# Kernel tuning notes

Measured on AMD Instinct MI355X. Metric: run time of the kernel, lower is better.

The kernel has to match this reference:

```python
import jax, jax.numpy as jnp
import numpy as np

# Module config (matches init_kwargs shape_data=[8,32,32], pow=1, spde_type='adv_diff')
N_T, N_Y, N_X = 8, 32, 32
N = N_Y * N_X            # nb_nodes
DX = DY = DT = 1.0


def build_A(kappa, m1, m2, h11, h12, h22):
    """Dense [N,N] advection-diffusion operator A = kappa^2 I + m.grad - div(H grad),
    central differences on the n_y x n_x grid, zero-Dirichlet boundary (9-pt stencil).
    All coefficient inputs are [N] vectors (node-wise)."""
    ii, jj = jnp.divmod(jnp.arange(N), N_X)   # ii: y index, jj: x index
    rows = jnp.arange(N)
    A = jnp.zeros((N, N), dtype=kappa.dtype)
    # center
    A = A.at[rows, rows].add(kappa ** 2 + 2.0 * h11 / DX**2 + 2.0 * h22 / DY**2)

    def add(A, di, dj, coef):
        vi, vj = ii + di, jj + dj
        valid = (vi >= 0) & (vi < N_Y) & (vj >= 0) & (vj < N_X)
        cols = jnp.clip(vi, 0, N_Y - 1) * N_X + jnp.clip(vj, 0, N_X - 1)
        return A.at[rows, cols].add(jnp.where(valid, coef, 0.0))

    A = add(A, 0, +1, -h11 / DX**2 + m1 / (2.0 * DX))
    A = add(A, 0, -1, -h11 / DX**2 - m1 / (2.0 * DX))
    A = add(A, +1, 0, -h22 / DY**2 + m2 / (2.0 * DY))
    A = add(A, -1, 0, -h22 / DY**2 - m2 / (2.0 * DY))
    cxy = h12 / (2.0 * DX * DY)    # cross term -2*H12*u_xy with /(4 dx dy) stencil
    A = add(A, +1, +1, -cxy)
    A = add(A, -1, -1, -cxy)
    A = add(A, +1, -1, +cxy)
    A = add(A, -1, +1, +cxy)
    return A


def _forward(kappa, m, H, tau):
    n_b = kappa.shape[0]
    # reorder field params to [n_b, n_t, N]
    kap = jnp.moveaxis(kappa[:, 0], -1, 1)
    m1 = jnp.moveaxis(m[:, 0], -1, 1)
    m2 = jnp.moveaxis(m[:, 1], -1, 1)
    h11 = jnp.moveaxis(H[:, 0, 0], -1, 1)
    h12 = jnp.moveaxis(H[:, 0, 1], -1, 1)
    h22 = jnp.moveaxis(H[:, 1, 1], -1, 1)
    tau_ = jnp.moveaxis(tau[:, 0], -1, 1)

    flat = lambda a: a.reshape(n_b * N_T, N)
    A = jax.vmap(build_A)(flat(kap), flat(m1), flat(m2), flat(h11), flat(h12), flat(h22))
    A = A.reshape(n_b, N_T, N, N)                 # B = A since pow == 1

    eye = jnp.eye(N, dtype=A.dtype)
    M = eye + DT * A                               # inv_M_k = I + dt*B_k, [n_b,n_t,N,N]
    w = DT / (tau_ ** 2)                           # Qs_tilde_k = diag(dt / tau_k^2)

    WM = w[..., :, None] * M                       # diag(w_k) @ M_k
    P = jnp.einsum('btij,btik->btjk', M, WM)       # M_k^T diag(w_k) M_k

    # diagonal blocks: D_k = P_k + diag(w_{k+1}) for k < n_t-1; D_{n_t-1} = P_{n_t-1}
    w_next = jnp.concatenate([w[:, 1:], jnp.zeros_like(w[:, :1])], axis=1)
    D = P + w_next[..., :, None] * eye

    # sub-diagonal block (k, k-1) = -M_k^T diag(w_k), k = 1..n_t-1 (0-block padded at front)
    zblk = jnp.zeros((n_b, 1, N, N), dtype=A.dtype)
    lower = jnp.concatenate([zblk, -jnp.swapaxes(WM[:, 1:], -1, -2)], axis=1)
    # super-diagonal block (k, k+1) = -diag(w_{k+1}) M_{k+1}, k = 0..n_t-2 (0-block at end)
    upper = jnp.concatenate([-WM[:, 1:], zblk], axis=1)

    # block-tridiagonal precision Q, packed as [n_b, 3(diag,lower,upper), n_t, N, N]
    return jnp.stack([D, lower, upper], axis=1)


def setup_inputs() -> dict:
    key = jax.random.key(0)
    ks = jax.random.split(key, 4)
    n_b = 2
    kappa = 0.1 + 0.9 * jax.random.uniform(ks[0], (n_b, 1, N, N_T), dtype=jnp.float32)
    m = 0.2 * jax.random.normal(ks[1], (n_b, 2, N, N_T), dtype=jnp.float32)
    H = jax.random.uniform(ks[2], (n_b, 2, 2, N, N_T), dtype=jnp.float32)
    H = H.at[:, 0, 1].multiply(0.2)
    H = H.at[:, 1, 0].set(H[:, 0, 1])              # symmetric diffusion tensor
    tau = 0.5 + jax.random.uniform(ks[3], (n_b, 1, N, N_T), dtype=jnp.float32)
    return {"kappa": kappa, "m": m, "H": H, "tau": tau}


def reference(kappa, m, H, tau):
    return _forward(kappa, m, H, tau)
```

## Files before the change

kernel.cpp:

```cpp
#include <hip/hip_runtime.h>

#define NT 8
#define NY 32
#define NX 32
#define NN 1024

typedef __attribute__((ext_vector_type(4))) float f32x4;

__device__ __forceinline__ void node_coefs(const float* __restrict__ kap,
                                           const float* __restrict__ m,
                                           const float* __restrict__ H,
                                           const float* __restrict__ tau,
                                           int b, int node, int tc,
                                           int iy, int ix,
                                           float* c , float& w) {
    const int base = node * NT + tc;
    const float kp  = kap[(b * NN) * NT + base];
    const float m1  = m[((b * 2 + 0) * NN) * NT + base];
    const float m2  = m[((b * 2 + 1) * NN) * NT + base];
    const float h11 = H[((b * 4 + 0) * NN) * NT + base];
    const float h12 = H[((b * 4 + 1) * NN) * NT + base];
    const float h22 = H[((b * 4 + 3) * NN) * NT + base];
    const float tv  = tau[(b * NN) * NT + base];
    w = 1.0f / (tv * tv);

    const float cxy = 0.5f * h12;
    const bool ym = iy > 0, yp = iy < NY - 1;
    const bool xm = ix > 0, xp = ix < NX - 1;

    c[4] = 1.0f + kp * kp + 2.0f * h11 + 2.0f * h22;
    c[0] = (ym && xm) ? -cxy               : 0.0f;
    c[1] =  ym        ? (-h22 - 0.5f * m2) : 0.0f;
    c[2] = (ym && xp) ?  cxy               : 0.0f;
    c[3] =  xm        ? (-h11 - 0.5f * m1) : 0.0f;
    c[5] =  xp        ? (-h11 + 0.5f * m1) : 0.0f;
    c[6] = (yp && xm) ?  cxy               : 0.0f;
    c[7] =  yp        ? (-h22 + 0.5f * m2) : 0.0f;
    c[8] = (yp && xp) ? -cxy               : 0.0f;
}

__device__ __forceinline__ void nt_store(f32x4* p, const float4& v) {
    __builtin_nontemporal_store(*(const f32x4*)&v, p);
}

__global__ __launch_bounds__(256) void spde_fused(const float* __restrict__ kap,
                                                  const float* __restrict__ m,
                                                  const float* __restrict__ H,
                                                  const float* __restrict__ tau,
                                                  float* __restrict__ out) {
    __shared__ float sc[3][18][9];
    __shared__ float sw[3][18];
    __shared__ float valsD[16][25];
    __shared__ float valsL[16][9];
    __shared__ float valsU[16][9];

    const int gb   = blockIdx.x;
    const int half = gb & 1;
    const int jy   = (gb >> 1) & 31;
    const int t    = (gb >> 6) & 7;
    const int b    = gb >> 9;
    const int jx0  = half * 16;
    const int tid  = threadIdx.x;

    if (tid < 54) {
        const int ly = tid / 18, lx = tid % 18;
        const int iy = jy + ly - 1, ix = jx0 + lx - 1;
        float c[9];
        float w = 0.0f;
        if (iy >= 0 && iy < NY && ix >= 0 && ix < NX) {
            node_coefs(kap, m, H, tau, b, iy * NX + ix, t, iy, ix, c, w);
        } else {
            #pragma unroll
            for (int q = 0; q < 9; ++q) c[q] = 0.0f;
        }
        #pragma unroll
        for (int q = 0; q < 9; ++q) sc[ly][lx][q] = c[q];
        sw[ly][lx] = w;
    }
    __syncthreads();

    #pragma unroll
    for (int pass = 0; pass < 3; ++pass) {
        const int e = tid + pass * 256;
        if (e < 400) {
            const int jj = e / 25, l = e % 25;
            const int dy = l / 5 - 2, dx = l % 5 - 2;
            float acc = 0.0f;
            #pragma unroll
            for (int d = 0; d < 9; ++d) {
                const int ey = d / 3 - 1, ex = d % 3 - 1;
                const int r2y = dy - ey, r2x = dx - ex;
                if (r2y >= -1 && r2y <= 1 && r2x >= -1 && r2x <= 1) {
                    const float* ci = sc[ey + 1][jj + 1 + ex];
                    acc += sw[ey + 1][jj + 1 + ex] * ci[8 - d]
                }
            }
            if (l == 12 && t < NT - 1) {
                const int j = jy * NX + jx0 + jj;
                const float tv = tau[((size_t)b * NN + j) * NT + (t + 1)];
                acc += 1.0f / (tv * tv);
            }
            valsD[jj][l] = acc;
        } else if (e < 544) {
            const int e2 = e - 400;
            const int jj = e2 / 9, d = e2 % 9;
            const int ey = d / 3 - 1, ex = d % 3 - 1;
            valsL[jj][d] = -sw[ey + 1][jj + 1 + ex] * sc[ey + 1][jj + 1 + ex][8 - d];
        } else if (e < 688) {
            const int e2 = e - 544;
            const int jj = e2 / 9, qi = e2 % 9;
            valsU[jj][qi] = -sw[1][jj + 1] * sc[1][jj + 1][qi];
        }
    }
    __syncthreads();

    const int q   = tid;
    const int ky  = q >> 3, kx0 = (q & 7) * 4;
    const int ddy = ky - jy;
    f32x4* const outq = (f32x4*)out;
    const size_t matD = ((size_t)(b * 3 + 0) * NT + t) << 18;
    const size_t matL = ((size_t)(b * 3 + 1) * NT + t) << 18;
    const int ut = (t >= 1) ? (t - 1) : 7;
    const size_t matU = ((size_t)(b * 3 + 2) * NT + ut) << 18;
    const bool inD  = (ddy >= -2 && ddy <= 2);
    const bool inLU = (ddy >= -1 && ddy <= 1);

    #pragma unroll 4
    for (int jj = 0; jj < 16; ++jj) {
        const int jx = jx0 + jj;
        const int j  = jy * NX + jx;
        const size_t rq = ((size_t)j << 8) + q;
        float4 vD = make_float4(0.f, 0.f, 0.f, 0.f);
        float4 vL = make_float4(0.f, 0.f, 0.f, 0.f);
        float4 vU = make_float4(0.f, 0.f, 0.f, 0.f);
        if (inD) {
            float* vp = &vD.x;
            const float* wrow = &valsD[jj][(ddy + 2) * 5 + 2];
            #pragma unroll
            for (int qq = 0; qq < 4; ++qq) {
                const int ddx = kx0 + qq - jx;
                if (ddx >= -2 && ddx <= 2) vp[qq] = wrow[ddx];
            }
        }
        if (inLU) {
            if (t > 0) {
                float* vp = &vL.x;
                const float* wrow = &valsL[jj][(ddy + 1) * 3 + 1];
                #pragma unroll
                for (int qq = 0; qq < 4; ++qq) {
                    const int ddx = kx0 + qq - jx;
                    if (ddx >= -1 && ddx <= 1) vp[qq] = wrow[ddx];
                }
            }
            if (t >= 1) {
                float* vp = &vU.x;
                const float* wrow = &valsU[jj][(ddy + 1) * 3 + 1];
                #pragma unroll
                for (int qq = 0; qq < 4; ++qq) {
                    const int ddx = kx0 + qq - jx;
                    if (ddx >= -1 && ddx <= 1) vp[qq] = wrow[ddx];
                }
            }
        }
        nt_store(outq + matD + rq, vD);
        nt_store(outq + matL + rq, vL);
        nt_store(outq + matU + rq, vU);
    }
}

extern "C" void kernel_launch(void* const* d_in, const int* in_sizes, int n_in,
                              void* d_out, int out_size, void* d_ws, size_t ws_size,
                              hipStream_t stream) {
    (void)n_in; (void)d_ws; (void)ws_size; (void)out_size;
    const float* kap = (const float*)d_in[0];
    const float* m   = (const float*)d_in[1];
    const float* H   = (const float*)d_in[2];
    const float* tau = (const float*)d_in[3];
    float* out = (float*)d_out;

    const int n_b = in_sizes[0] / (NN * NT);
    const int grid = n_b * NT * NY * 2;
    spde_fused<<<grid, 256, 0, stream>>>(kap, m, H, tau, out);
}
```

Measured before the change: 212.8 us.

## Zero output with memset and scatter only band entries per grid row

Replaces the kernel that wrote every element of the dense output with a device memset followed by a kernel that writes only the nonzero stencil bands. Each block now handles a full grid row instead of half a row. The intent is to let a bulk fill produce the zeros at higher bandwidth than per-thread nontemporal stores. The scatter kernel writes far fewer bytes, in exchange for an extra launch and scattered partial writes.

New measurement: 191.0 us. 10.3% less time.

```diff
diff --git a/kernel.cpp b/kernel.cpp
--- a/kernel.cpp
+++ b/kernel.cpp
@@ -39,32 +39,26 @@
     c[8] = (yp && xp) ? -cxy               : 0.0f;
 }
 
-__device__ __forceinline__ void nt_store(f32x4* p, const float4& v) {
-    __builtin_nontemporal_store(*(const f32x4*)&v, p);
-}
+__global__ __launch_bounds__(256) void spde_scatter_row(const float* __restrict__ kap,
+                                                        const float* __restrict__ m,
+                                                        const float* __restrict__ H,
+                                                        const float* __restrict__ tau,
+                                                        float* __restrict__ out) {
+    __shared__ float sc[3][34][9];
+    __shared__ float sw[3][34];
+    __shared__ float valsD[32][25];
+    __shared__ float valsL[32][9];
+    __shared__ float valsU[32][9];
 
-__global__ __launch_bounds__(256) void spde_fused(const float* __restrict__ kap,
-                                                  const float* __restrict__ m,
-                                                  const float* __restrict__ H,
-                                                  const float* __restrict__ tau,
-                                                  float* __restrict__ out) {
-    __shared__ float sc[3][18][9];
-    __shared__ float sw[3][18];
-    __shared__ float valsD[16][25];
-    __shared__ float valsL[16][9];
-    __shared__ float valsU[16][9];
+    const int gb  = blockIdx.x;
+    const int jy  = gb & 31;
+    const int t   = (gb >> 5) & 7;
+    const int b   = gb >> 8;
+    const int tid = threadIdx.x;
 
-    const int gb   = blockIdx.x;
-    const int half = gb & 1;
-    const int jy   = (gb >> 1) & 31;
-    const int t    = (gb >> 6) & 7;
-    const int b    = gb >> 9;
-    const int jx0  = half * 16;
-    const int tid  = threadIdx.x;
-
-    if (tid < 54) {
-        const int ly = tid / 18, lx = tid % 18;
-        const int iy = jy + ly - 1, ix = jx0 + lx - 1;
+    if (tid < 102) {
+        const int ly = tid / 34, lx = tid % 34;
+        const int iy = jy + ly - 1, ix = lx - 1;
         float c[9];
         float w = 0.0f;
         if (iy >= 0 && iy < NY && ix >= 0 && ix < NX) {
@@ -80,9 +74,9 @@
     __syncthreads();
 
     #pragma unroll
-    for (int pass = 0; pass < 3; ++pass) {
+    for (int pass = 0; pass < 6; ++pass) {
         const int e = tid + pass * 256;
-        if (e < 400) {
+        if (e < 800) {
             const int jj = e / 25, l = e % 25;
             const int dy = l / 5 - 2, dx = l % 5 - 2;
             float acc = 0.0f;
@@ -96,82 +90,87 @@
                 }
             }
             if (l == 12 && t < NT - 1) {
-                const int j = jy * NX + jx0 + jj;
+                const int j = jy * NX + jj;
                 const float tv = tau[((size_t)b * NN + j) * NT + (t + 1)];
                 acc += 1.0f / (tv * tv);
             }
             valsD[jj][l] = acc;
-        } else if (e < 544) {
-            const int e2 = e - 400;
+        } else if (e < 1088) {
+            const int e2 = e - 800;
             const int jj = e2 / 9, d = e2 % 9;
             const int ey = d / 3 - 1, ex = d % 3 - 1;
             valsL[jj][d] = -sw[ey + 1][jj + 1 + ex] * sc[ey + 1][jj + 1 + ex][8 - d];
-        } else if (e < 688) {
-            const int e2 = e - 544;
+        } else if (e < 1376) {
+            const int e2 = e - 1088;
             const int jj = e2 / 9, qi = e2 % 9;
             valsU[jj][qi] = -sw[1][jj + 1] * sc[1][jj + 1][qi];
         }
     }
     __syncthreads();
 
-    const int q   = tid;
-    const int ky  = q >> 3, kx0 = (q & 7) * 4;
-    const int ddy = ky - jy;
     f32x4* const outq = (f32x4*)out;
     const size_t matD = ((size_t)(b * 3 + 0) * NT + t) << 18;
-    const size_t matL = ((size_t)(b * 3 + 1) * NT + t) << 18;
-    const int ut = (t >= 1) ? (t - 1) : 7;
-    const size_t matU = ((size_t)(b * 3 + 2) * NT + ut) << 18;
-    const bool inD  = (ddy >= -2 && ddy <= 2);
-    const bool inLU = (ddy >= -1 && ddy <= 1);
+    const int rowbase = jy * NX;
 
-    #pragma unroll 4
-    for (int jj = 0; jj < 16; ++jj) {
-        const int jx = jx0 + jj;
-        const int j  = jy * NX + jx;
-        const size_t rq = ((size_t)j << 8) + q;
-        float4 vD = make_float4(0.f, 0.f, 0.f, 0.f);
-        float4 vL = make_float4(0.f, 0.f, 0.f, 0.f);
-        float4 vU = make_float4(0.f, 0.f, 0.f, 0.f);
-        if (inD) {
-            float* vp = &vD.x;
-            const float* wrow = &valsD[jj][(ddy + 2) * 5 + 2];
+    #pragma unroll
+    for (int pass = 0; pass < 5; ++pass) {
+        const int idx = tid + pass * 256;
+        const int jj = idx / 40, r = idx % 40;
+        const int s = r >> 3, q = r & 7;
+        const int ky = jy - 2 + s;
+        if (ky >= 0 && ky < NY) {
+            f32x4 v = {0.f, 0.f, 0.f, 0.f};
             #pragma unroll
-            for (int qq = 0; qq < 4; ++qq) {
-                const int ddx = kx0 + qq - jx;
-                if (ddx >= -2 && ddx <= 2) vp[qq] = wrow[ddx];
+            for (int cq = 0; cq < 4; ++cq) {
+                const int ddx = q * 4 + cq - jj;
+                if (ddx >= -2 && ddx <= 2) v[cq] = valsD[jj][s * 5 + (ddx + 2)];
+            }
+            outq[matD + ((size_t)(rowbase + jj) << 8) + ky * 8 + q] = v;
+        }
+    }
+
+    if (t >= 1) {
+        const size_t matL = ((size_t)(b * 3 + 1) * NT + t) << 18;
+        const size_t matU = ((size_t)(b * 3 + 2) * NT + (t - 1)) << 18;
+        #pragma unroll
+        for (int pass = 0; pass < 3; ++pass) {
+            const int idx = tid + pass * 256;
+            const int jj = idx / 24, r = idx % 24;
+            const int s = r >> 3, q = r & 7;
+            const int ky = jy - 1 + s;
+            if (ky >= 0 && ky < NY) {
+                f32x4 v = {0.f, 0.f, 0.f, 0.f};
+                #pragma unroll
+                for (int cq = 0; cq < 4; ++cq) {
+                    const int ddx = q * 4 + cq - jj;
+                    if (ddx >= -1 && ddx <= 1) v[cq] = valsL[jj][s * 3 + (ddx + 1)];
+                }
+                outq[matL + ((size_t)(rowbase + jj) << 8) + ky * 8 + q] = v;
             }
         }
-        if (inLU) {
-            if (t > 0) {
-                float* vp = &vL.x;
-                const float* wrow = &valsL[jj][(ddy + 1) * 3 + 1];
+        #pragma unroll
+        for (int pass = 0; pass < 3; ++pass) {
+            const int idx = tid + pass * 256;
+            const int jj = idx / 24, r = idx % 24;
+            const int s = r >> 3, q = r & 7;
+            const int ky = jy - 1 + s;
+            if (ky >= 0 && ky < NY) {
+                f32x4 v = {0.f, 0.f, 0.f, 0.f};
                 #pragma unroll
-                for (int qq = 0; qq < 4; ++qq) {
-                    const int ddx = kx0 + qq - jx;
-                    if (ddx >= -1 && ddx <= 1) vp[qq] = wrow[ddx];
+                for (int cq = 0; cq < 4; ++cq) {
+                    const int ddx = q * 4 + cq - jj;
+                    if (ddx >= -1 && ddx <= 1) v[cq] = valsU[jj][s * 3 + (ddx + 1)];
                 }
-            }
-            if (t >= 1) {
-                float* vp = &vU.x;
-                const float* wrow = &valsU[jj][(ddy + 1) * 3 + 1];
-                #pragma unroll
-                for (int qq = 0; qq < 4; ++qq) {
-                    const int ddx = kx0 + qq - jx;
-                    if (ddx >= -1 && ddx <= 1) vp[qq] = wrow[ddx];
-                }
+                outq[matU + ((size_t)(rowbase + jj) << 8) + ky * 8 + q] = v;
             }
         }
-        nt_store(outq + matD + rq, vD);
-        nt_store(outq + matL + rq, vL);
-        nt_store(outq + matU + rq, vU);
     }
 }
 
 extern "C" void kernel_launch(void* const* d_in, const int* in_sizes, int n_in,
                               void* d_out, int out_size, void* d_ws, size_t ws_size,
                               hipStream_t stream) {
-    (void)n_in; (void)d_ws; (void)ws_size; (void)out_size;
+    (void)n_in; (void)d_ws; (void)ws_size;
     const float* kap = (const float*)d_in[0];
     const float* m   = (const float*)d_in[1];
     const float* H   = (const float*)d_in[2];
@@ -179,6 +178,9 @@
     float* out = (float*)d_out;
 
     const int n_b = in_sizes[0] / (NN * NT);
-    const int grid = n_b * NT * NY * 2;
-    spde_fused<<<grid, 256, 0, stream>>>(kap, m, H, tau, out);
+
+    hipMemsetAsync(d_out, 0, (size_t)out_size, stream);
+
+    const int grid = n_b * NT * NY;
+    spde_scatter_row<<<grid, 256, 0, stream>>>(kap, m, H, tau, out);
 }
```
